# Optimization experiments

Measured on AMD Instinct MI355X. Metric: run time of the kernel, lower is better.

Reference implementation:

```python
import jax, jax.numpy as jnp
import numpy as np

B, S, E = 1, 2048, 2048
HQ, HKV = 32, 8
D = E // HQ            # 64 head dim
REP = HQ // HKV        # 4 q-heads per kv-head
NEG = -1e9


def _rope(t, fr, fi):
    # t: [B,S,H,D]; fr/fi: [S,D//2] real/imag of unit complex freqs
    tr = t.reshape(*t.shape[:-1], D // 2, 2)
    t0, t1 = tr[..., 0], tr[..., 1]
    fr = fr[None, :, None, :]
    fi = fi[None, :, None, :]
    out = jnp.stack([t0 * fr - t1 * fi, t0 * fi + t1 * fr], axis=-1)
    return out.reshape(t.shape)


def setup_inputs() -> dict:
    key = jax.random.key(0)
    kx, kq, kk, kv, ko = jax.random.split(key, 5)
    x = jax.random.normal(kx, (B, S, E), dtype=jnp.float32)
    # standard RoPE frequencies: theta = 10000^{-2i/D}
    inv_freq = 1.0 / (10000.0 ** (np.arange(0, D, 2, dtype=np.float32) / D))
    ang = np.arange(S, dtype=np.float32)[:, None] * inv_freq[None, :]  # [S, D//2]
    freqs_cis = jnp.asarray(np.stack([np.cos(ang), np.sin(ang)], axis=-1))  # [S,D//2,2]
    # causal additive mask [S,S]
    mask = jnp.where(np.tril(np.ones((S, S), dtype=bool)), 0.0, NEG).astype(jnp.float32)
    s = 1.0 / np.sqrt(E)
    Wq = jax.random.normal(kq, (E, HQ * D), dtype=jnp.float32) * s
    Wk = jax.random.normal(kk, (E, HKV * D), dtype=jnp.float32) * s
    Wv = jax.random.normal(kv, (E, HKV * D), dtype=jnp.float32) * s
    Wo = jax.random.normal(ko, (HQ * D, E), dtype=jnp.float32) * s
    return {"x": x, "freqs_cis": freqs_cis, "mask": mask,
            "Wq": Wq, "Wk": Wk, "Wv": Wv, "Wo": Wo}


def reference(x, freqs_cis, mask, Wq, Wk, Wv, Wo):
    b, s, _ = x.shape
    xq = (x @ Wq).reshape(b, s, HQ, D)
    xk = (x @ Wk).reshape(b, s, HKV, D)
    xv = (x @ Wv).reshape(b, s, HKV, D)
    fr, fi = freqs_cis[..., 0], freqs_cis[..., 1]
    xq = _rope(xq, fr, fi)
    xk = _rope(xk, fr, fi)
    # explicit GQA kv-head repeat (matches torch repeat+view)
    xk = jnp.repeat(xk, REP, axis=2)  # [b,s,HQ,D]
    xv = jnp.repeat(xv, REP, axis=2)
    q = xq.transpose(0, 2, 1, 3)  # [b,h,s,d]
    k = xk.transpose(0, 2, 1, 3)
    v = xv.transpose(0, 2, 1, 3)
    scores = jnp.einsum('bhqd,bhkd->bhqk', q, k) / jnp.sqrt(jnp.float32(D))
    scores = scores + mask[None, None]
    probs = jax.nn.softmax(scores, axis=-1)
    attn = jnp.einsum('bhqk,bhkd->bhqd', probs, v)
    attn = attn.transpose(0, 2, 1, 3).reshape(b, s, HQ * D)
    return attn @ Wo
```

## Files before the change

### kernel.cpp

```cpp
#include <hip/hip_runtime.h>
#include <stdint.h>

#define SEQ   2048
#define EDIM  2048
#define NHQ   32
#define NHKV  8
#define HDIM  64
#define NQKV  3072

#define LOG2E 1.4426950408889634f

typedef __bf16 bf16x8 __attribute__((ext_vector_type(8)));
typedef float  f32x4  __attribute__((ext_vector_type(4)));

typedef __attribute__((address_space(1))) void gvoid;
typedef __attribute__((address_space(3))) void lvoid;

__device__ __forceinline__ unsigned short f2bf(float f) {
  unsigned int u = __builtin_bit_cast(unsigned int, f);
  u += 0x7FFFu + ((u >> 16) & 1u);
  return (unsigned short)(u >> 16);
}

__device__ __forceinline__ unsigned int pk2bf(float lo, float hi) {
  return (unsigned)f2bf(lo) | ((unsigned)f2bf(hi) << 16);
}

__device__ __forceinline__ float fexp2(float x) {
#if __has_builtin(__builtin_amdgcn_exp2f)
  return __builtin_amdgcn_exp2f(x);
#else
  return exp2f(x);
#endif
}

__device__ __forceinline__ bf16x8 ld_g16(const unsigned short* p) {
  uint4 u = *reinterpret_cast<const uint4*>(p);
  return __builtin_bit_cast(bf16x8, u);
}

__device__ __forceinline__ void stage16(const void* g, void* l) {
  __builtin_amdgcn_global_load_lds((gvoid*)g, (lvoid*)l, 16, 0, 0);
}

__global__ __launch_bounds__(256) void conv_x_kernel(
    const float* __restrict__ x, unsigned short* __restrict__ xb) {
  int i = (blockIdx.x * 256 + threadIdx.x) * 8;
  float4 a = *reinterpret_cast<const float4*>(x + i);
  float4 b = *reinterpret_cast<const float4*>(x + i + 4);
  uint4 o;
  o.x = pk2bf(a.x, a.y);
  o.y = pk2bf(a.z, a.w);
  o.z = pk2bf(b.x, b.y);
  o.w = pk2bf(b.z, b.w);
  *reinterpret_cast<uint4*>(xb + i) = o;
}

__global__ __launch_bounds__(256) void tr_qkv_kernel(
    const float* __restrict__ Wq, const float* __restrict__ Wk,
    const float* __restrict__ Wv, unsigned short* __restrict__ Bt) {
  __shared__ float tile[32][33];
  const int tx = threadIdx.x, ty = threadIdx.y;
  const int kb = blockIdx.x * 32, nb = blockIdx.y * 32;
#pragma unroll
  for (int i = 0; i < 4; ++i) {
    int k = kb + ty + i * 8;
    int n = nb + tx;
    float v;
    if (n < 2048)      v = Wq[k * 2048 + n];
    else if (n < 2560) v = Wk[k * 512 + (n - 2048)];
    else               v = Wv[k * 512 + (n - 2560)];
    tile[ty + i * 8][tx] = v;
  }
  __syncthreads();
#pragma unroll
  for (int i = 0; i < 4; ++i) {
    int n = nb + ty + i * 8;
    int k = kb + tx;
    Bt[n * 2048 + k] = f2bf(tile[tx][ty + i * 8]);
  }
}

__global__ __launch_bounds__(256) void tr_wo_kernel(
    const float* __restrict__ Wo, unsigned short* __restrict__ Bt) {
  __shared__ float tile[32][33];
  const int tx = threadIdx.x, ty = threadIdx.y;
  const int kb = blockIdx.x * 32, nb = blockIdx.y * 32;
#pragma unroll
  for (int i = 0; i < 4; ++i)
    tile[ty + i * 8][tx] = Wo[(kb + ty + i * 8) * 2048 + nb + tx];
  __syncthreads();
#pragma unroll
  for (int i = 0; i < 4; ++i)
    Bt[(nb + ty + i * 8) * 2048 + kb + tx] = f2bf(tile[tx][ty + i * 8]);
}

template <int MODE>
__global__ __launch_bounds__(256) void gemm_kernel(
    const unsigned short* __restrict__ A, const unsigned short* __restrict__ Bt,
    const float* __restrict__ freqs, unsigned short* __restrict__ Qb,
    unsigned short* __restrict__ Kb, unsigned short* __restrict__ VT,
    float* __restrict__ Cout, int N_, int K, int nwg) {
  __shared__ alignas(16) unsigned short As[2][128 * 64];
  __shared__ alignas(16) unsigned short Bs[2][64 * 64];
  const int t = threadIdx.x;
  const int w = t >> 6, l = t & 63;
  const int q = l >> 4, r16 = l & 15;
  const int wr = w >> 1, wc = w & 1;
  const int cpx = nwg >> 3;
  const int id = (blockIdx.x & 7) * cpx + (blockIdx.x >> 3);
  const int brow = (id & 15) * 128;
  const int bcol = (id >> 4) * 64;
  const unsigned short* Arow = A + (size_t)brow * K;
  const unsigned short* Brow = Bt + (size_t)bcol * K;
  f32x4 acc[4][2] = {};

#define STAGE_TILE(buf, ktb)                                                  \
  {                                                                           \
    _Pragma("unroll") for (int it = 0; it < 4; ++it) {                        \
      int sg = it * 256 + t;                                                  \
      int row = sg >> 3, ks = sg & 7;                                         \
      stage16(Arow + (size_t)row * K + (ktb) + ((ks ^ (row & 7)) << 3),       \
              (char*)As[buf] + sg * 16);                                      \
    }                                                                         \
    _Pragma("unroll") for (int it = 0; it < 2; ++it) {                        \
      int sg = it * 256 + t;                                                  \
      int row = sg >> 3, ks = sg & 7;                                         \
      stage16(Brow + (size_t)row * K + (ktb) + ((ks ^ (row & 7)) << 3),       \
              (char*)Bs[buf] + sg * 16);                                      \
    }                                                                         \
  }

  STAGE_TILE(0, 0)
  __syncthreads();

  for (int kt = 0; kt < K; kt += 64) {
    const int cur = (kt >> 6) & 1;
    if (kt + 64 < K) STAGE_TILE(cur ^ 1, kt + 64)
#pragma unroll
    for (int kk = 0; kk < 2; ++kk) {
      bf16x8 af[4], bfr[2];
#pragma unroll
      for (int mf = 0; mf < 4; ++mf) {
        int arow = wr * 64 + mf * 16 + r16;
        int slot = ((kk << 2) + q) ^ (arow & 7);
        af[mf] = *(const bf16x8*)(As[cur] + arow * 64 + slot * 8);
      }
#pragma unroll
      for (int nf = 0; nf < 2; ++nf) {
        int brw = wc * 32 + nf * 16 + r16;
        int slot = ((kk << 2) + q) ^ (brw & 7);
        bfr[nf] = *(const bf16x8*)(Bs[cur] + brw * 64 + slot * 8);
      }
#pragma unroll
      for (int mf = 0; mf < 4; ++mf)
#pragma unroll
        for (int nf = 0; nf < 2; ++nf)
          acc[mf][nf] = __builtin_amdgcn_mfma_f32_16x16x32_bf16(
              af[mf], bfr[nf], acc[mf][nf], 0, 0, 0);
    }
    __syncthreads();
  }

#pragma unroll
  for (int mf = 0; mf < 4; ++mf) {
#pragma unroll
    for (int nf = 0; nf < 2; ++nf) {
      int j = bcol + wc * 32 + nf * 16 + r16;
#pragma unroll
      for (int reg = 0; reg < 4; ++reg) {
        float v = acc[mf][nf][reg];
        int srow = brow + wr * 64 + mf * 16 + q * 4 + reg;
        if (MODE == 1) {
          Cout[(size_t)srow * N_ + j] = v;
        } else {
          float pv = __shfl_xor(v, 1);
          int d = j & 63;
          if (j < 2048) {
            float2 f = *reinterpret_cast<const float2*>(
                freqs + ((size_t)srow * 32 + (d >> 1)) * 2);
            float ov = (d & 1) ? (pv * f.y + v * f.x) : (v * f.x - pv * f.y);
            Qb[(size_t)(j >> 6) * (SEQ * HDIM) + srow * HDIM + d] =
                f2bf(ov * (0.125f * LOG2E));
          } else if (j < 2560) {
            float2 f = *reinterpret_cast<const float2*>(
                freqs + ((size_t)srow * 32 + (d >> 1)) * 2);
            float ov = (d & 1) ? (pv * f.y + v * f.x) : (v * f.x - pv * f.y);
            Kb[(size_t)((j - 2048) >> 6) * (SEQ * HDIM) + srow * HDIM + d] =
                f2bf(ov);
          } else {
            VT[(size_t)((j - 2560) >> 6) * (HDIM * SEQ) + d * SEQ + srow] =
                f2bf(v);
          }
        }
      }
    }
  }
#undef STAGE_TILE
}

__global__ __launch_bounds__(64, 3) void flash_kernel(
    const unsigned short* __restrict__ Qb, const unsigned short* __restrict__ Kb,
    const unsigned short* __restrict__ VT, unsigned short* __restrict__ attnb) {
  const int bi = blockIdx.x;
  const int h = bi & 31, hk = h >> 2;
  const int qc = 63 - (bi >> 5);
  const int l = threadIdx.x & 63;
  const int hi = l >> 4, r16 = l & 15;
  const int qrow0 = qc * 32;
  const unsigned short* Qh = Qb + (size_t)h * (SEQ * HDIM);
  const unsigned short* Kh = Kb + (size_t)hk * (SEQ * HDIM);
  const unsigned short* Vh = VT + (size_t)hk * (HDIM * SEQ);

  bf16x8 qf[2][2];
#pragma unroll
  for (int mf = 0; mf < 2; ++mf)
#pragma unroll
    for (int ks = 0; ks < 2; ++ks)
      qf[mf][ks] = ld_g16(Qh + (qrow0 + mf * 16 + r16) * HDIM + ks * 32 + hi * 8);

  f32x4 o[2][4] = {};
  float mrow[2] = {-1e9f, -1e9f};
  float lrow[2] = {0.f, 0.f};

  const int nkv = (qc >> 2) + 1;
  for (int kv = 0; kv < nkv; ++kv) {
    const int kvbase = kv * 128;
    f32x4 s[2][8] = {};
#pragma unroll
    for (int nf = 0; nf < 8; ++nf) {
      const unsigned short* kp =
          Kh + (size_t)(kvbase + nf * 16 + r16) * HDIM + hi * 8;
      bf16x8 a0 = ld_g16(kp);
      bf16x8 a1 = ld_g16(kp + 32);
      s[0][nf] = __builtin_amdgcn_mfma_f32_16x16x32_bf16(a0, qf[0][0], s[0][nf], 0, 0, 0);
      s[1][nf] = __builtin_amdgcn_mfma_f32_16x16x32_bf16(a0, qf[1][0], s[1][nf], 0, 0, 0);
      s[0][nf] = __builtin_amdgcn_mfma_f32_16x16x32_bf16(a1, qf[0][1], s[0][nf], 0, 0, 0);
      s[1][nf] = __builtin_amdgcn_mfma_f32_16x16x32_bf16(a1, qf[1][1], s[1][nf], 0, 0, 0);
    }
    if (kv == nkv - 1) {
#pragma unroll
      for (int mf = 0; mf < 2; ++mf) {
        int qr = qrow0 + mf * 16 + r16;
#pragma unroll
        for (int nf = 0; nf < 8; ++nf) {
          int kc = kvbase + nf * 16 + hi * 4;
#pragma unroll
          for (int r = 0; r < 4; ++r)
            if (kc + r > qr) s[mf][nf][r] = -1e9f;
        }
      }
    }
    float mx[2];
#pragma unroll
    for (int mf = 0; mf < 2; ++mf) {
      f32x4 m4 = s[mf][0];
#pragma unroll
      for (int nf = 1; nf < 8; ++nf) {
        m4[0] = fmaxf(m4[0], s[mf][nf][0]); m4[1] = fmaxf(m4[1], s[mf][nf][1]);
        m4[2] = fmaxf(m4[2], s[mf][nf][2]); m4[3] = fmaxf(m4[3], s[mf][nf][3]);
      }
      float v = fmaxf(fmaxf(m4[0], m4[1]), fmaxf(m4[2], m4[3]));
      v = fmaxf(v, __shfl_xor(v, 16));
      v = fmaxf(v, __shfl_xor(v, 32));
      mx[mf] = v;
    }
    if (!__all(fmaxf(mx[0] - mrow[0], mx[1] - mrow[1]) <= 8.0f)) {
#pragma unroll
      for (int mf = 0; mf < 2; ++mf) {
        float mn = fmaxf(mrow[mf], mx[mf]);
        float al = fexp2(mrow[mf] - mn);
        mrow[mf] = mn;
        lrow[mf] *= al;
#pragma unroll
        for (int r = 0; r < 4; ++r) {
          float alr = __shfl(al, hi * 4 + r);
#pragma unroll
          for (int nd = 0; nd < 4; ++nd) o[mf][nd][r] *= alr;
        }
      }
    }
#pragma unroll
    for (int mf = 0; mf < 2; ++mf) {
      f32x4 a4 = {0.f, 0.f, 0.f, 0.f};
#pragma unroll
      for (int nf = 0; nf < 8; ++nf) {
#pragma unroll
        for (int r = 0; r < 4; ++r) {
          float p = fexp2(s[mf][nf][r] - mrow[mf]);
          s[mf][nf][r] = p;
          a4[r] += p;
        }
      }
      float rs = (a4[0] + a4[1]) + (a4[2] + a4[3]);
      rs += __shfl_xor(rs, 16);
      rs += __shfl_xor(rs, 32);
      lrow[mf] += rs;
    }
#pragma unroll
    for (int kt = 0; kt < 8; ++kt) {
      bf16x8 pa[2];
#pragma unroll
      for (int mf = 0; mf < 2; ++mf) {
        bf16x8 p = {};
        p[0] = (__bf16)s[mf][kt][0];
        p[1] = (__bf16)s[mf][kt][1];
        p[2] = (__bf16)s[mf][kt][2];
        p[3] = (__bf16)s[mf][kt][3];
        pa[mf] = p;
      }
#pragma unroll
      for (int nd = 0; nd < 4; ++nd) {
        uint2 v2 = *reinterpret_cast<const uint2*>(
            Vh + (size_t)(nd * 16 + r16) * SEQ + kvbase + kt * 16 + hi * 4);
        uint4 u; u.x = v2.x; u.y = v2.y; u.z = 0u; u.w = 0u;
        bf16x8 vb = __builtin_bit_cast(bf16x8, u);
        o[0][nd] = __builtin_amdgcn_mfma_f32_16x16x32_bf16(pa[0], vb, o[0][nd], 0, 0, 0);
        o[1][nd] = __builtin_amdgcn_mfma_f32_16x16x32_bf16(pa[1], vb, o[1][nd], 0, 0, 0);
      }
    }
  }
#pragma unroll
  for (int mf = 0; mf < 2; ++mf) {
    float linv = 1.0f / lrow[mf];
#pragma unroll
    for (int r = 0; r < 4; ++r) {
      float lr = __shfl(linv, hi * 4 + r);
      int srow = qrow0 + mf * 16 + hi * 4 + r;
#pragma unroll
      for (int nd = 0; nd < 4; ++nd) {
        int d = nd * 16 + r16;
        attnb[(size_t)srow * 2048 + h * 64 + d] = f2bf(o[mf][nd][r] * lr);
      }
    }
  }
}

extern "C" void kernel_launch(void* const* d_in, const int* in_sizes, int n_in,
                              void* d_out, int out_size, void* d_ws,
                              size_t ws_size, hipStream_t stream) {
  const float* x     = (const float*)d_in[0];
  const float* freqs = (const float*)d_in[1];
  const float* Wq = (const float*)d_in[3];
  const float* Wk = (const float*)d_in[4];
  const float* Wv = (const float*)d_in[5];
  const float* Wo = (const float*)d_in[6];
  float* out = (float*)d_out;
  char* ws = (char*)d_ws;
  const size_t MB = 1024 * 1024;
  unsigned short* xb    = (unsigned short*)(ws);
  unsigned short* WqkvT = (unsigned short*)(ws + 8 * MB);
  unsigned short* WoT   = (unsigned short*)(ws + 20 * MB);
  unsigned short* Qbuf  = (unsigned short*)(ws + 28 * MB);
  unsigned short* Kbuf  = (unsigned short*)(ws + 36 * MB);
  unsigned short* Vt    = (unsigned short*)(ws + 38 * MB);
  unsigned short* attnb = (unsigned short*)(ws + 40 * MB);

  conv_x_kernel<<<dim3(2048), dim3(256), 0, stream>>>(x, xb);
  tr_qkv_kernel<<<dim3(64, 96), dim3(32, 8), 0, stream>>>(Wq, Wk, Wv, WqkvT);
  tr_wo_kernel<<<dim3(64, 64), dim3(32, 8), 0, stream>>>(Wo, WoT);
  gemm_kernel<0><<<dim3(768), dim3(256), 0, stream>>>(
      xb, WqkvT, freqs, Qbuf, Kbuf, Vt, (float*)nullptr, NQKV, 2048, 768);
  flash_kernel<<<dim3(2048), dim3(64), 0, stream>>>(Qbuf, Kbuf, Vt, attnb);
  gemm_kernel<1><<<dim3(512), dim3(256), 0, stream>>>(
      attnb, WoT, (const float*)nullptr, (unsigned short*)nullptr,
      (unsigned short*)nullptr, (unsigned short*)nullptr, out, 2048, 2048, 512);
}
```

Before: 325.8 us.

## Prefetch next K tile into registers and batch V loads before softmax

```diff
diff --git a/kernel.cpp b/kernel.cpp
--- a/kernel.cpp
+++ b/kernel.cpp
@@ -199,7 +199,7 @@
 #undef STAGE_TILE
 }
 
-__global__ __launch_bounds__(64, 3) void flash_kernel(
+__global__ __launch_bounds__(64, 2) void flash_kernel(
     const unsigned short* __restrict__ Qb, const unsigned short* __restrict__ Kb,
     const unsigned short* __restrict__ VT, unsigned short* __restrict__ attnb) {
   const int bi = blockIdx.x;
@@ -224,20 +224,42 @@
   float lrow[2] = {0.f, 0.f};
 
   const int nkv = (qc >> 2) + 1;
+
+  bf16x8 k0[8], k1[8];
+  const unsigned short* kbase = Kh + (size_t)r16 * HDIM + hi * 8;
+#pragma unroll
+  for (int nf = 0; nf < 8; ++nf) {
+    const unsigned short* kp = kbase + (size_t)(nf * 16) * HDIM;
+    k0[nf] = ld_g16(kp);
+    k1[nf] = ld_g16(kp + 32);
+  }
+
   for (int kv = 0; kv < nkv; ++kv) {
     const int kvbase = kv * 128;
     f32x4 s[2][8] = {};
 #pragma unroll
     for (int nf = 0; nf < 8; ++nf) {
-      const unsigned short* kp =
-          Kh + (size_t)(kvbase + nf * 16 + r16) * HDIM + hi * 8;
-      bf16x8 a0 = ld_g16(kp);
-      bf16x8 a1 = ld_g16(kp + 32);
-      s[0][nf] = __builtin_amdgcn_mfma_f32_16x16x32_bf16(a0, qf[0][0], s[0][nf], 0, 0, 0);
-      s[1][nf] = __builtin_amdgcn_mfma_f32_16x16x32_bf16(a0, qf[1][0], s[1][nf], 0, 0, 0);
-      s[0][nf] = __builtin_amdgcn_mfma_f32_16x16x32_bf16(a1, qf[0][1], s[0][nf], 0, 0, 0);
-      s[1][nf] = __builtin_amdgcn_mfma_f32_16x16x32_bf16(a1, qf[1][1], s[1][nf], 0, 0, 0);
-    }
+      s[0][nf] = __builtin_amdgcn_mfma_f32_16x16x32_bf16(k0[nf], qf[0][0], s[0][nf], 0, 0, 0);
+      s[1][nf] = __builtin_amdgcn_mfma_f32_16x16x32_bf16(k0[nf], qf[1][0], s[1][nf], 0, 0, 0);
+      s[0][nf] = __builtin_amdgcn_mfma_f32_16x16x32_bf16(k1[nf], qf[0][1], s[0][nf], 0, 0, 0);
+      s[1][nf] = __builtin_amdgcn_mfma_f32_16x16x32_bf16(k1[nf], qf[1][1], s[1][nf], 0, 0, 0);
+    }
+    if (kv + 1 < nkv) {
+      const unsigned short* kp2 = kbase + (size_t)(kvbase + 128) * HDIM;
+#pragma unroll
+      for (int nf = 0; nf < 8; ++nf) {
+        const unsigned short* kp = kp2 + (size_t)(nf * 16) * HDIM;
+        k0[nf] = ld_g16(kp);
+        k1[nf] = ld_g16(kp + 32);
+      }
+    }
+    uint2 vv[4][8];
+#pragma unroll
+    for (int nd = 0; nd < 4; ++nd)
+#pragma unroll
+      for (int kt = 0; kt < 8; ++kt)
+        vv[nd][kt] = *reinterpret_cast<const uint2*>(
+            Vh + (size_t)(nd * 16 + r16) * SEQ + kvbase + kt * 16 + hi * 4);
     if (kv == nkv - 1) {
 #pragma unroll
       for (int mf = 0; mf < 2; ++mf) {
@@ -311,9 +333,7 @@
       }
 #pragma unroll
       for (int nd = 0; nd < 4; ++nd) {
-        uint2 v2 = *reinterpret_cast<const uint2*>(
-            Vh + (size_t)(nd * 16 + r16) * SEQ + kvbase + kt * 16 + hi * 4);
-        uint4 u; u.x = v2.x; u.y = v2.y; u.z = 0u; u.w = 0u;
+        uint4 u; u.x = vv[nd][kt].x; u.y = vv[nd][kt].y; u.z = 0u; u.w = 0u;
         bf16x8 vb = __builtin_bit_cast(bf16x8, u);
         o[0][nd] = __builtin_amdgcn_mfma_f32_16x16x32_bf16(pa[0], vb, o[0][nd], 0, 0, 0);
         o[1][nd] = __builtin_amdgcn_mfma_f32_16x16x32_bf16(pa[1], vb, o[1][nd], 0, 0, 0);
```

New measurement: 346.3 us. +6.3%, slower.
